# Kernel tuning notes

Hardware: AMD Instinct MI355X
Metric: run time of the kernel (lower is better)

Reference implementation:

```python
import jax, jax.numpy as jnp
import numpy as np

EMBED = 512
HEADS = 8
HEAD_DIM = EMBED // HEADS
SCALE_BASE = 512
NEG = -1e9


def xpos_apply(x, offset, downscale):
    # x: [(b h), L, d]
    L, d = x.shape[1], x.shape[2]
    min_pos = -(L + offset) // 2
    max_pos = L + offset + min_pos
    base = (jnp.arange(0, d, 2, dtype=jnp.float32) + 0.4 * d) / (1.4 * d)      # [d/2]
    power = jnp.arange(min_pos, max_pos, dtype=jnp.float32) / SCALE_BASE        # [L']
    scale = base[None, :] ** power[:, None]                                     # [L', d/2]
    half = d // 2
    inv_freq = 1.0 / (10000.0 ** (jnp.arange(half, dtype=jnp.float32) / half))
    sinusoid = jnp.arange(scale.shape[0], dtype=jnp.float32)[:, None] * inv_freq[None, :]
    sin, cos = jnp.sin(sinusoid), jnp.cos(sinusoid)
    # keep last L rows (no-op when offset == 0)
    scale, sin, cos = scale[-L:], sin[-L:], cos[-L:]
    if downscale:
        scale = 1.0 / scale
    sin2 = jnp.repeat(sin * scale, 2, axis=-1)   # duplicate_interleave -> [L, d]
    cos2 = jnp.repeat(cos * scale, 2, axis=-1)
    x1, x2 = x[..., ::2], x[..., 1::2]
    rot = jnp.stack([-x2, x1], axis=-1).reshape(x.shape)  # rotate_every_two
    return x * cos2[None] + rot * sin2[None]


def split_heads(x, b, L):
    # 'b l (h d) -> (b h) l d'
    return x.reshape(b, L, HEADS, HEAD_DIM).transpose(0, 2, 1, 3).reshape(b * HEADS, L, HEAD_DIM)


def setup_inputs() -> dict:
    key = jax.random.key(0)
    ks = jax.random.split(key, 12)
    b, L = 4, 2048
    inp = {
        'query': jax.random.normal(ks[0], (b, L, EMBED), jnp.float32),
        'key': jax.random.normal(ks[1], (b, L, EMBED), jnp.float32),
        'value': jax.random.normal(ks[2], (b, L, EMBED), jnp.float32),
        'key_padding_mask': jnp.zeros((b, L), jnp.bool_),
        'attn_mask': jnp.where(jnp.tril(jnp.ones((L, L), jnp.bool_)), 0.0, NEG).astype(jnp.float32),
    }
    s = 1.0 / np.sqrt(EMBED)
    inp['Wq'] = jax.random.normal(ks[3], (EMBED, EMBED), jnp.float32) * s
    inp['bq'] = jnp.zeros((EMBED,), jnp.float32)
    inp['Wk'] = jax.random.normal(ks[4], (EMBED, EMBED), jnp.float32) * s
    inp['bk'] = jnp.zeros((EMBED,), jnp.float32)
    inp['Wv'] = jax.random.normal(ks[5], (EMBED, EMBED), jnp.float32) * s
    inp['bv'] = jnp.zeros((EMBED,), jnp.float32)
    inp['Wo'] = jax.random.normal(ks[6], (EMBED, EMBED), jnp.float32) * s
    inp['bo'] = jnp.zeros((EMBED,), jnp.float32)
    return inp


def reference(query, key, value, key_padding_mask, attn_mask, Wq, bq, Wk, bk, Wv, bv, Wo, bo):
    b, L, _ = query.shape
    q = split_heads(query @ Wq.T + bq, b, L)
    k = split_heads(key @ Wk.T + bk, b, L)
    v = split_heads(value @ Wv.T + bv, b, L)
    k = xpos_apply(k, 0, True)
    q = xpos_apply(q, 0, False)
    q = q * (HEAD_DIM ** -0.5)
    aw = jnp.einsum('btd,bsd->bts', q, k)                 # [(b h), t, s]
    aw = jnp.nan_to_num(aw) + attn_mask[None]
    aw = aw.reshape(b, HEADS, L, L)
    aw = jnp.where(key_padding_mask[:, None, None, :], jnp.finfo(aw.dtype).min, aw)
    aw = aw.reshape(b * HEADS, L, L)
    probs = jax.nn.softmax(aw.astype(jnp.float32), axis=-1).astype(aw.dtype)
    attn = jnp.einsum('bts,bsd->btd', probs, v)           # [(b h), t, d]
    attn = attn.reshape(b, HEADS, L, HEAD_DIM).transpose(0, 2, 1, 3).reshape(b, L, EMBED)
    return attn @ Wo.T + bo
```

## Files before the change

kernel.cpp:

```cpp
#include <hip/hip_runtime.h>
#include <hip/hip_bf16.h>

typedef __bf16 bf16x2 __attribute__((ext_vector_type(2)));
typedef __bf16 bf16x4 __attribute__((ext_vector_type(4)));
typedef __bf16 bf16x8 __attribute__((ext_vector_type(8)));
typedef float  f32x4  __attribute__((ext_vector_type(4)));

#define SEQ    2048
#define EMB    512
#define NHEAD  8
#define HD     64
#define NBATCH 4
#define MROWS  (NBATCH*SEQ)
#define QSCALE 0.18033688011112042f
#define INV2PI 0.15915494309189535f
#define TWOPI  6.28318530717958648f
#define NEGFREQ (-0.41524101186092028f)

__device__ __forceinline__ f32x4 mfma16(bf16x8 a, bf16x8 b, f32x4 c) {
  return __builtin_amdgcn_mfma_f32_16x16x32_bf16(a, b, c, 0, 0, 0);
}

typedef __attribute__((address_space(1))) const void gv_t;
typedef __attribute__((address_space(3))) void lv_t;
__device__ __forceinline__ void async16(const void* g, void* l) {
  __builtin_amdgcn_global_load_lds((gv_t*)g, (lv_t*)l, 16, 0, 0);
}

__global__ __launch_bounds__(256) void conv_kernel(const float* __restrict__ q,
                                                   const float* __restrict__ k,
                                                   const float* __restrict__ v,
                                                   __bf16* __restrict__ Qf,
                                                   __bf16* __restrict__ Kf,
                                                   __bf16* __restrict__ Vf) {
  const int z = blockIdx.y;
  const float* src = (z == 0) ? q : (z == 1) ? k : v;
  __bf16* dst = (z == 0) ? Qf : (z == 1) ? Kf : Vf;
  const size_t i8 = ((size_t)blockIdx.x * 256 + threadIdx.x) * 8;
  const float4 fa = ((const float4*)(src + i8))[0];
  const float4 fb = ((const float4*)(src + i8))[1];
  bf16x8 h = { (__bf16)fa.x, (__bf16)fa.y, (__bf16)fa.z, (__bf16)fa.w,
               (__bf16)fb.x, (__bf16)fb.y, (__bf16)fb.z, (__bf16)fb.w };
  *(bf16x8*)(dst + i8) = h;
}

__device__ __forceinline__ void gemm_main(const __bf16* __restrict__ A,
                                          const float* __restrict__ W,
                                          __bf16* As, __bf16* Bs,
                                          f32x4 (&acc)[4][4], int m0, int n0) {
  const int tid = threadIdx.x;
  const int wid = tid >> 6, lane = tid & 63;
  const int quad = lane >> 4, l16 = lane & 15;
  const int srow = lane >> 3;
  const int sxor = ((lane & 7) ^ srow) * 8;
  const int wm = (wid >> 1) * 64, wn = (wid & 1) * 64;

  #pragma unroll
  for (int i = 0; i < 4; ++i)
    #pragma unroll
    for (int j = 0; j < 4; ++j) acc[i][j] = (f32x4)(0.0f);

  for (int k0 = 0; k0 < 512; k0 += 64) {
    __syncthreads();
    #pragma unroll
    for (int ii = 0; ii < 4; ++ii) {
      const int r8 = wid * 32 + ii * 8;
      async16(A + (size_t)(m0 + r8 + srow) * 512 + k0 + sxor, &As[r8 * 64]);
    }
    {
      const int row = tid >> 1, c0 = (tid & 1) << 5;
      const float* src = W + (size_t)(n0 + row) * 512 + k0 + c0;
      __bf16* dst = Bs + row * 72 + c0;
      #pragma unroll
      for (int j = 0; j < 4; ++j) {
        const float4 fa = ((const float4*)src)[2 * j];
        const float4 fb = ((const float4*)src)[2 * j + 1];
        bf16x8 h = { (__bf16)fa.x, (__bf16)fa.y, (__bf16)fa.z, (__bf16)fa.w,
                     (__bf16)fb.x, (__bf16)fb.y, (__bf16)fb.z, (__bf16)fb.w };
        *((bf16x8*)(dst + 8 * j)) = h;
      }
    }
    __syncthreads();
    #pragma unroll
    for (int ks = 0; ks < 2; ++ks) {
      bf16x8 af[4], bfr[4];
      #pragma unroll
      for (int i = 0; i < 4; ++i)
        af[i] = *(const bf16x8*)&As[(wm + i * 16 + l16) * 64 +
                                    (((quad + ks * 4) ^ (l16 & 7)) * 8)];
      #pragma unroll
      for (int j = 0; j < 4; ++j)
        bfr[j] = *(const bf16x8*)&Bs[(wn + j * 16 + l16) * 72 + ks * 32 + quad * 8];
      #pragma unroll
      for (int i = 0; i < 4; ++i)
        #pragma unroll
        for (int j = 0; j < 4; ++j)
          acc[i][j] = mfma16(af[i], bfr[j], acc[i][j]);
    }
  }
}

__global__ __launch_bounds__(256) void gemm_proj_kernel(
    const __bf16* __restrict__ Qf, const __bf16* __restrict__ Kf, const __bf16* __restrict__ Vf,
    const float* __restrict__ wq, const float* __restrict__ wk, const float* __restrict__ wv,
    const float* __restrict__ bq, const float* __restrict__ bk, const float* __restrict__ bv,
    __bf16* __restrict__ Qx, __bf16* __restrict__ Kx, __bf16* __restrict__ Vt) {
  __shared__ __align__(16) char smem[34816];
  __bf16* As = (__bf16*)smem;
  __bf16* Bs = (__bf16*)(smem + 16384);
  __bf16* T  = (__bf16*)smem;

  const int z = blockIdx.z;
  const __bf16* A = (z == 0) ? Qf : (z == 1) ? Kf : Vf;
  const float* W  = (z == 0) ? wq : (z == 1) ? wk : wv;
  const float* bias = (z == 0) ? bq : (z == 1) ? bk : bv;
  const int m0 = blockIdx.y * 128, n0 = blockIdx.x * 128;

  f32x4 acc[4][4];
  gemm_main(A, W, As, Bs, acc, m0, n0);

  const int tid = threadIdx.x;
  const int wid = tid >> 6, lane = tid & 63;
  const int quad = lane >> 4, l16 = lane & 15;
  const int wm = (wid >> 1) * 64, wn = (wid & 1) * 64;

  __syncthreads();

  if (z == 2) {
    #pragma unroll
    for (int j = 0; j < 4; ++j) {
      const float bval = bias[n0 + wn + j * 16 + l16];
      #pragma unroll
      for (int i = 0; i < 4; ++i) {
        bf16x4 p = { (__bf16)(acc[i][j][0] + bval), (__bf16)(acc[i][j][1] + bval),
                     (__bf16)(acc[i][j][2] + bval), (__bf16)(acc[i][j][3] + bval) };
        *(bf16x4*)&T[(wn + j * 16 + l16) * 136 + wm + i * 16 + quad * 4] = p;
      }
    }
    __syncthreads();
    const int nrow = tid >> 1, mh = (tid & 1) << 6;
    bf16x8 vv[8];
    #pragma unroll
    for (int u = 0; u < 8; ++u) vv[u] = *(const bf16x8*)&T[nrow * 136 + mh + u * 8];
    const int n = n0 + nrow, h = n >> 6, d = n & 63;
    const int bb = m0 >> 11, lb2 = (m0 & 2047) + mh;
    __bf16* dst = Vt + ((size_t)(bb * 8 + h) * 64 + d) * 2048 + lb2;
    #pragma unroll
    for (int u = 0; u < 8; ++u) *(bf16x8*)(dst + u * 8) = vv[u];
  } else {
    #pragma unroll
    for (int j = 0; j < 4; ++j) {
      const float bval = bias[n0 + wn + j * 16 + l16];
      #pragma unroll
      for (int i = 0; i < 4; ++i)
        #pragma unroll
        for (int r = 0; r < 4; ++r)
          T[(wm + i * 16 + quad * 4 + r) * 136 + wn + j * 16 + l16] =
              (__bf16)(acc[i][j][r] + bval);
    }
    __syncthreads();
    const int lrow = tid >> 1, half = tid & 1;
    const int gm = m0 + lrow, l = gm & 2047, bb = gm >> 11;
    const int h = (n0 >> 6) + half;
    bf16x8 vv[8];
    #pragma unroll
    for (int u = 0; u < 8; ++u)
      vv[u] = *(const bf16x8*)&T[lrow * 136 + half * 64 + u * 8];
    bf16x8 ov[8];
    const float lf = (float)l;
    const float pw = (lf - 1024.0f) * (1.0f / 512.0f);
    const float qs = (z == 0) ? QSCALE : 1.0f;
    #pragma unroll
    for (int i = 0; i < 32; ++i) {
      const float x1 = (float)vv[i >> 2][(2 * i) & 7];
      const float x2 = (float)vv[i >> 2][(2 * i + 1) & 7];
      const float lb = __log2f((2.0f * i + 25.6f) * (1.0f / 89.6f));
      const float e  = (z == 0) ? (pw * lb) : (-pw * lb);
      const float sc = __builtin_amdgcn_exp2f(e) * qs;
      const float ang = lf * __builtin_amdgcn_exp2f((float)i * NEGFREQ);
      float rev = ang * INV2PI;
      rev -= floorf(rev);
      const float ar = rev * TWOPI;
      const float sn = __sinf(ar) * sc;
      const float cs = __cosf(ar) * sc;
      ov[i >> 2][(2 * i) & 7]     = (__bf16)(x1 * cs - x2 * sn);
      ov[i >> 2][(2 * i + 1) & 7] = (__bf16)(x2 * cs + x1 * sn);
    }
    __bf16* dst = ((z == 0) ? Qx : Kx) + ((size_t)(bb * 8 + h) * 2048 + l) * 64;
    #pragma unroll
    for (int u = 0; u < 8; ++u) *(bf16x8*)(dst + u * 8) = ov[u];
  }
}

__global__ __launch_bounds__(256) void gemm_out_kernel(
    const __bf16* __restrict__ A, const float* __restrict__ W,
    const float* __restrict__ bias, float* __restrict__ C) {
  __shared__ __align__(16) char smem[34816];
  __bf16* As = (__bf16*)smem;
  __bf16* Bs = (__bf16*)(smem + 16384);
  const int m0 = blockIdx.y * 128, n0 = blockIdx.x * 128;
  f32x4 acc[4][4];
  gemm_main(A, W, As, Bs, acc, m0, n0);
  const int tid = threadIdx.x;
  const int wid = tid >> 6, lane = tid & 63;
  const int quad = lane >> 4, l16 = lane & 15;
  const int wm = (wid >> 1) * 64, wn = (wid & 1) * 64;
  #pragma unroll
  for (int j = 0; j < 4; ++j) {
    const int n = n0 + wn + j * 16 + l16;
    const float bval = bias[n];
    #pragma unroll
    for (int i = 0; i < 4; ++i)
      #pragma unroll
      for (int r = 0; r < 4; ++r)
        C[(size_t)(m0 + wm + i * 16 + quad * 4 + r) * 512 + n] = acc[i][j][r] + bval;
  }
}

__global__ __launch_bounds__(256, 3) void flash_kernel(const __bf16* __restrict__ Qx,
                                                       const __bf16* __restrict__ Kx,
                                                       const __bf16* __restrict__ Vt,
                                                       const unsigned char* __restrict__ kpm,
                                                       __bf16* __restrict__ Oa) {
  __shared__ __align__(16) __bf16 Qs[128 * HD];
  __shared__ __align__(16) __bf16 Ks[64 * HD];
  __shared__ __align__(16) __bf16 Vs[64 * HD];
  __shared__ __align__(16) __bf16 Ps[4][32 * 72];
  __shared__ __align__(16) unsigned char kpmS[2048];

  const int tid = threadIdx.x;
  const int wid = tid >> 6;
  const int lane = tid & 63;
  const int quad = lane >> 4;
  const int l16 = lane & 15;
  const int l7 = l16 & 7;
  const int srow = lane >> 3;
  const int sxor = ((lane & 7) ^ srow) * 8;
  const int bh = blockIdx.x;
  const int b = bh >> 3, h = bh & 7;
  const int y = blockIdx.y;
  const int qt = (y < 8) ? (15 - y) : (y - 8);
  const int q0 = qt * 128;
  const int nkv = 2 * qt + 2;

  const __bf16* Qbase = Qx + (size_t)bh * (SEQ * HD);
  const __bf16* Kbase = Kx + (size_t)bh * (SEQ * HD);
  const __bf16* Vbase = Vt + (size_t)bh * (HD * SEQ);
  __bf16* Pw = &Ps[wid][0];

  #pragma unroll
  for (int ii = 0; ii < 4; ++ii) {
    const int r0 = wid * 32 + ii * 8;
    async16(Qbase + (size_t)(q0 + r0 + srow) * HD + sxor, &Qs[r0 * HD]);
  }
  if (wid < 2) async16(kpm + b * SEQ + tid * 16, &kpmS[tid * 16]);
  #pragma unroll
  for (int ii = 0; ii < 2; ++ii) {
    const int r0 = wid * 16 + ii * 8;
    async16(Kbase + (size_t)(r0 + srow) * HD + sxor, &Ks[r0 * HD]);
    async16(Vbase + (size_t)(r0 + srow) * SEQ + sxor, &Vs[r0 * HD]);
  }
  __syncthreads();

  bf16x8 qf[2][2];
  #pragma unroll
  for (int ks = 0; ks < 2; ++ks)
    #pragma unroll
    for (int c = 0; c < 2; ++c)
      qf[ks][c] = *(const bf16x8*)&Qs[(wid * 32 + c * 16 + l16) * HD +
                                      (((quad + ks * 4) ^ l7) * 8)];

  f32x4 o[4][2];
  #pragma unroll
  for (int db = 0; db < 4; ++db)
    #pragma unroll
    for (int c = 0; c < 2; ++c) o[db][c] = (f32x4)(0.0f);
  float m_run[2] = { -3.0e38f, -3.0e38f };
  float l_run[2] = { 0.0f, 0.0f };
  const int myq0 = q0 + wid * 32 + l16;

  for (int kvt = 0; kvt < nkv; ++kvt) {
    f32x4 s[4][2];
    #pragma unroll
    for (int nb = 0; nb < 4; ++nb)
      #pragma unroll
      for (int c = 0; c < 2; ++c) s[nb][c] = (f32x4)(0.0f);
    #pragma unroll
    for (int ks = 0; ks < 2; ++ks) {
      bf16x8 kf[4];
      #pragma unroll
      for (int nb = 0; nb < 4; ++nb)
        kf[nb] = *(const bf16x8*)&Ks[(nb * 16 + l16) * HD + (((quad + ks * 4) ^ l7) * 8)];
      #pragma unroll
      for (int nb = 0; nb < 4; ++nb)
        #pragma unroll
        for (int c = 0; c < 2; ++c)
          s[nb][c] = mfma16(kf[nb], qf[ks][c], s[nb][c]);
    }

    if (kvt * 64 + 63 > q0 + wid * 32) {
      #pragma unroll
      for (int c = 0; c < 2; ++c) {
        const int myq = myq0 + c * 16;
        #pragma unroll
        for (int nb = 0; nb < 4; ++nb)
          #pragma unroll
          for (int r = 0; r < 4; ++r)
            if (kvt * 64 + nb * 16 + quad * 4 + r > myq) s[nb][c][r] = -1e30f;
      }
    }
    #pragma unroll
    for (int nb = 0; nb < 4; ++nb) {
      const unsigned pk = *(const unsigned*)&kpmS[kvt * 64 + nb * 16 + quad * 4];
      if (pk) {
        #pragma unroll
        for (int c = 0; c < 2; ++c) {
          if (pk & 0x000000FFu) s[nb][c][0] = -1e30f;
          if (pk & 0x0000FF00u) s[nb][c][1] = -1e30f;
          if (pk & 0x00FF0000u) s[nb][c][2] = -1e30f;
          if (pk & 0xFF000000u) s[nb][c][3] = -1e30f;
        }
      }
    }

    float alpha[2];
    #pragma unroll
    for (int c = 0; c < 2; ++c) {
      float mx = s[0][c][0];
      #pragma unroll
      for (int nb = 0; nb < 4; ++nb)
        #pragma unroll
        for (int r = 0; r < 4; ++r) mx = fmaxf(mx, s[nb][c][r]);
      mx = fmaxf(mx, __shfl_xor(mx, 16));
      mx = fmaxf(mx, __shfl_xor(mx, 32));
      const float m_new = fmaxf(m_run[c], mx);
      alpha[c] = __builtin_amdgcn_exp2f(m_run[c] - m_new);
      m_run[c] = m_new;
      float ssum = 0.0f;
      #pragma unroll
      for (int nb = 0; nb < 4; ++nb) {
        #pragma unroll
        for (int r = 0; r < 4; ++r) {
          const float p = __builtin_amdgcn_exp2f(s[nb][c][r] - m_new);
          s[nb][c][r] = p;
          ssum += p;
        }
      }
      ssum += __shfl_xor(ssum, 16);
      ssum += __shfl_xor(ssum, 32);
      l_run[c] = l_run[c] * alpha[c] + ssum;
    }

    #pragma unroll
    for (int c = 0; c < 2; ++c)
      #pragma unroll
      for (int nb = 0; nb < 4; ++nb) {
        bf16x4 p4 = { (__bf16)s[nb][c][0], (__bf16)s[nb][c][1],
                      (__bf16)s[nb][c][2], (__bf16)s[nb][c][3] };
        *(bf16x4*)&Pw[(c * 16 + l16) * 72 + nb * 16 + quad * 4] = p4;
      }
    #pragma unroll
    for (int db = 0; db < 4; ++db)
      #pragma unroll
      for (int c = 0; c < 2; ++c) o[db][c] *= alpha[c];

    #pragma unroll
    for (int ks = 0; ks < 2; ++ks) {
      bf16x8 pf[2];
      #pragma unroll
      for (int c = 0; c < 2; ++c)
        pf[c] = *(const bf16x8*)&Pw[(c * 16 + l16) * 72 + ks * 32 + quad * 8];
      #pragma unroll
      for (int db = 0; db < 4; ++db) {
        const bf16x8 vf = *(const bf16x8*)&Vs[(db * 16 + l16) * HD +
                                              (((quad + ks * 4) ^ l7) * 8)];
        #pragma unroll
        for (int c = 0; c < 2; ++c)
          o[db][c] = mfma16(vf, pf[c], o[db][c]);
      }
    }

    __syncthreads();
    if (kvt + 1 < nkv) {
      const int kvn = kvt + 1;
      #pragma unroll
      for (int ii = 0; ii < 2; ++ii) {
        const int r0 = wid * 16 + ii * 8;
        async16(Kbase + (size_t)(kvn * 64 + r0 + srow) * HD + sxor, &Ks[r0 * HD]);
        async16(Vbase + (size_t)(r0 + srow) * SEQ + kvn * 64 + sxor, &Vs[r0 * HD]);
      }
    }
    __syncthreads();
  }

  #pragma unroll
  for (int c = 0; c < 2; ++c) {
    const float inv_l = 1.0f / l_run[c];
    #pragma unroll
    for (int db = 0; db < 4; ++db) {
      bf16x4 t4 = { (__bf16)(o[db][c][0] * inv_l), (__bf16)(o[db][c][1] * inv_l),
                    (__bf16)(o[db][c][2] * inv_l), (__bf16)(o[db][c][3] * inv_l) };
      *(bf16x4*)&Pw[(c * 16 + l16) * 72 + db * 16 + quad * 4] = t4;
    }
  }
  #pragma unroll
  for (int ii = 0; ii < 4; ++ii) {
    const int qr = ii * 8 + srow;
    const bf16x8 ovv = *(const bf16x8*)&Pw[qr * 72 + (lane & 7) * 8];
    *(bf16x8*)(Oa + (((size_t)b * SEQ + q0 + wid * 32 + qr) * NHEAD + h) * HD +
               (lane & 7) * 8) = ovv;
  }
}

extern "C" void kernel_launch(void* const* d_in, const int* in_sizes, int n_in,
                              void* d_out, int out_size, void* d_ws, size_t ws_size,
                              hipStream_t stream) {
  (void)in_sizes; (void)n_in; (void)out_size; (void)ws_size;
  const float* query = (const float*)d_in[0];
  const float* key   = (const float*)d_in[1];
  const float* value = (const float*)d_in[2];
  const unsigned char* kpm = (const unsigned char*)d_in[3];
  const float* Wq = (const float*)d_in[5];
  const float* bq = (const float*)d_in[6];
  const float* Wk = (const float*)d_in[7];
  const float* bk = (const float*)d_in[8];
  const float* Wv = (const float*)d_in[9];
  const float* bv = (const float*)d_in[10];
  const float* Wo = (const float*)d_in[11];
  const float* bo = (const float*)d_in[12];
  float* out = (float*)d_out;

  char* ws = (char*)d_ws;
  const size_t SZ = (size_t)MROWS * EMB * 2;
  __bf16* Qf = (__bf16*)(ws);
  __bf16* Kf = (__bf16*)(ws + SZ);
  __bf16* Vf = (__bf16*)(ws + 2 * SZ);
  __bf16* Qx = (__bf16*)(ws + 3 * SZ);
  __bf16* Kx = (__bf16*)(ws + 4 * SZ);
  __bf16* Vt = (__bf16*)(ws + 5 * SZ);
  __bf16* Oa = Qf;

  conv_kernel<<<dim3(2048, 3), dim3(256), 0, stream>>>(query, key, value, Qf, Kf, Vf);
  gemm_proj_kernel<<<dim3(4, 64, 3), dim3(256), 0, stream>>>(
      Qf, Kf, Vf, Wq, Wk, Wv, bq, bk, bv, Qx, Kx, Vt);
  flash_kernel<<<dim3(32, 16), dim3(256), 0, stream>>>(Qx, Kx, Vt, kpm, Oa);
  gemm_out_kernel<<<dim3(4, 64), dim3(256), 0, stream>>>(Oa, Wo, bo, out);
}
```

Measured before the change: 239.3 us.

## Split flash attention into single-wave blocks reading K/V directly from global

Replaces the 4-wave block with shared-memory K/V staging by single-wavefront blocks, each handling two 32-row query tiles paired from opposite ends of the causal range so work per block is balanced. K, V, Q and the padding mask are now loaded straight from global memory into registers, with no LDS staging and no block barriers. This removes synchronization and LDS copies and raises the block count, but K/V tiles are no longer shared across waves, so global/L2 traffic rises and global loads go unswizzled and non-prefetched. It also drops the async double-load overlap.

```diff
diff --git a/kernel.cpp b/kernel.cpp
--- a/kernel.cpp
+++ b/kernel.cpp
@@ -217,198 +217,170 @@
   }
 }
 
-__global__ __launch_bounds__(256, 3) void flash_kernel(const __bf16* __restrict__ Qx,
-                                                       const __bf16* __restrict__ Kx,
-                                                       const __bf16* __restrict__ Vt,
-                                                       const unsigned char* __restrict__ kpm,
-                                                       __bf16* __restrict__ Oa) {
-  __shared__ __align__(16) __bf16 Qs[128 * HD];
-  __shared__ __align__(16) __bf16 Ks[64 * HD];
-  __shared__ __align__(16) __bf16 Vs[64 * HD];
-  __shared__ __align__(16) __bf16 Ps[4][32 * 72];
-  __shared__ __align__(16) unsigned char kpmS[2048];
-
-  const int tid = threadIdx.x;
-  const int wid = tid >> 6;
-  const int lane = tid & 63;
+__global__ __launch_bounds__(64) void flash_kernel(const __bf16* __restrict__ Qx,
+                                                   const __bf16* __restrict__ Kx,
+                                                   const __bf16* __restrict__ Vt,
+                                                   const unsigned char* __restrict__ kpm,
+                                                   __bf16* __restrict__ Oa) {
+  __shared__ __align__(16) __bf16 Pw[32 * 72];
+
+  const int lane = threadIdx.x;
   const int quad = lane >> 4;
   const int l16 = lane & 15;
-  const int l7 = l16 & 7;
-  const int srow = lane >> 3;
-  const int sxor = ((lane & 7) ^ srow) * 8;
   const int bh = blockIdx.x;
   const int b = bh >> 3, h = bh & 7;
-  const int y = blockIdx.y;
-  const int qt = (y < 8) ? (15 - y) : (y - 8);
-  const int q0 = qt * 128;
-  const int nkv = 2 * qt + 2;
+  const int w = blockIdx.y;
 
   const __bf16* Qbase = Qx + (size_t)bh * (SEQ * HD);
   const __bf16* Kbase = Kx + (size_t)bh * (SEQ * HD);
   const __bf16* Vbase = Vt + (size_t)bh * (HD * SEQ);
-  __bf16* Pw = &Ps[wid][0];
-
-  #pragma unroll
-  for (int ii = 0; ii < 4; ++ii) {
-    const int r0 = wid * 32 + ii * 8;
-    async16(Qbase + (size_t)(q0 + r0 + srow) * HD + sxor, &Qs[r0 * HD]);
-  }
-  if (wid < 2) async16(kpm + b * SEQ + tid * 16, &kpmS[tid * 16]);
-  #pragma unroll
-  for (int ii = 0; ii < 2; ++ii) {
-    const int r0 = wid * 16 + ii * 8;
-    async16(Kbase + (size_t)(r0 + srow) * HD + sxor, &Ks[r0 * HD]);
-    async16(Vbase + (size_t)(r0 + srow) * SEQ + sxor, &Vs[r0 * HD]);
-  }
-  __syncthreads();
-
-  bf16x8 qf[2][2];
-  #pragma unroll
-  for (int ks = 0; ks < 2; ++ks)
-    #pragma unroll
-    for (int c = 0; c < 2; ++c)
-      qf[ks][c] = *(const bf16x8*)&Qs[(wid * 32 + c * 16 + l16) * HD +
-                                      (((quad + ks * 4) ^ l7) * 8)];
-
-  f32x4 o[4][2];
-  #pragma unroll
-  for (int db = 0; db < 4; ++db)
-    #pragma unroll
-    for (int c = 0; c < 2; ++c) o[db][c] = (f32x4)(0.0f);
-  float m_run[2] = { -3.0e38f, -3.0e38f };
-  float l_run[2] = { 0.0f, 0.0f };
-  const int myq0 = q0 + wid * 32 + l16;
-
-  for (int kvt = 0; kvt < nkv; ++kvt) {
-    f32x4 s[4][2];
-    #pragma unroll
-    for (int nb = 0; nb < 4; ++nb)
-      #pragma unroll
-      for (int c = 0; c < 2; ++c) s[nb][c] = (f32x4)(0.0f);
-    #pragma unroll
-    for (int ks = 0; ks < 2; ++ks) {
-      bf16x8 kf[4];
+  const unsigned char* kpb = kpm + b * SEQ;
+
+  #pragma unroll 1
+  for (int phase = 0; phase < 2; ++phase) {
+    const int qb2 = phase ? w : (63 - w);
+    const int q0 = qb2 * 32;
+    const int nkv = (qb2 >> 1) + 1;
+
+    bf16x8 qf[2][2];
+    #pragma unroll
+    for (int ks = 0; ks < 2; ++ks)
+      #pragma unroll
+      for (int c = 0; c < 2; ++c)
+        qf[ks][c] = *(const bf16x8*)(Qbase + (size_t)(q0 + c * 16 + l16) * HD +
+                                     ks * 32 + quad * 8);
+
+    f32x4 o[4][2];
+    #pragma unroll
+    for (int db = 0; db < 4; ++db)
+      #pragma unroll
+      for (int c = 0; c < 2; ++c) o[db][c] = (f32x4)(0.0f);
+    float m_run[2] = { -3.0e38f, -3.0e38f };
+    float l_run[2] = { 0.0f, 0.0f };
+
+    #pragma unroll 1
+    for (int kvt = 0; kvt < nkv; ++kvt) {
+      const int kv0 = kvt * 64;
+
+      f32x4 s[4][2];
       #pragma unroll
       for (int nb = 0; nb < 4; ++nb)
-        kf[nb] = *(const bf16x8*)&Ks[(nb * 16 + l16) * HD + (((quad + ks * 4) ^ l7) * 8)];
-      #pragma unroll
-      for (int nb = 0; nb < 4; ++nb)
+        #pragma unroll
+        for (int c = 0; c < 2; ++c) s[nb][c] = (f32x4)(0.0f);
+      #pragma unroll
+      for (int ks = 0; ks < 2; ++ks) {
+        bf16x8 kf[4];
+        #pragma unroll
+        for (int nb = 0; nb < 4; ++nb)
+          kf[nb] = *(const bf16x8*)(Kbase + (size_t)(kv0 + nb * 16 + l16) * HD +
+                                    ks * 32 + quad * 8);
+        #pragma unroll
+        for (int nb = 0; nb < 4; ++nb)
+          #pragma unroll
+          for (int c = 0; c < 2; ++c)
+            s[nb][c] = mfma16(kf[nb], qf[ks][c], s[nb][c]);
+      }
+
+      if (kvt == nkv - 1) {
+        #pragma unroll
+        for (int c = 0; c < 2; ++c) {
+          const int myq = q0 + c * 16 + l16;
+          #pragma unroll
+          for (int nb = 0; nb < 4; ++nb)
+            #pragma unroll
+            for (int r = 0; r < 4; ++r)
+              if (kv0 + nb * 16 + quad * 4 + r > myq) s[nb][c][r] = -1e30f;
+        }
+      }
+      #pragma unroll
+      for (int nb = 0; nb < 4; ++nb) {
+        const unsigned pk = *(const unsigned*)(kpb + kv0 + nb * 16 + quad * 4);
+        if (pk) {
+          #pragma unroll
+          for (int c = 0; c < 2; ++c) {
+            if (pk & 0x000000FFu) s[nb][c][0] = -1e30f;
+            if (pk & 0x0000FF00u) s[nb][c][1] = -1e30f;
+            if (pk & 0x00FF0000u) s[nb][c][2] = -1e30f;
+            if (pk & 0xFF000000u) s[nb][c][3] = -1e30f;
+          }
+        }
+      }
+
+      float alpha[2];
+      #pragma unroll
+      for (int c = 0; c < 2; ++c) {
+        float mx = s[0][c][0];
+        #pragma unroll
+        for (int nb = 0; nb < 4; ++nb)
+          #pragma unroll
+          for (int r = 0; r < 4; ++r) mx = fmaxf(mx, s[nb][c][r]);
+        mx = fmaxf(mx, __shfl_xor(mx, 16));
+        mx = fmaxf(mx, __shfl_xor(mx, 32));
+        const float m_new = fmaxf(m_run[c], mx);
+        alpha[c] = __builtin_amdgcn_exp2f(m_run[c] - m_new);
+        m_run[c] = m_new;
+        float ssum = 0.0f;
+        #pragma unroll
+        for (int nb = 0; nb < 4; ++nb) {
+          #pragma unroll
+          for (int r = 0; r < 4; ++r) {
+            const float p = __builtin_amdgcn_exp2f(s[nb][c][r] - m_new);
+            s[nb][c][r] = p;
+            ssum += p;
+          }
+        }
+        ssum += __shfl_xor(ssum, 16);
+        ssum += __shfl_xor(ssum, 32);
+        l_run[c] = l_run[c] * alpha[c] + ssum;
+      }
+
+      #pragma unroll
+      for (int c = 0; c < 2; ++c)
+        #pragma unroll
+        for (int nb = 0; nb < 4; ++nb) {
+          bf16x4 p4 = { (__bf16)s[nb][c][0], (__bf16)s[nb][c][1],
+                        (__bf16)s[nb][c][2], (__bf16)s[nb][c][3] };
+          *(bf16x4*)&Pw[(c * 16 + l16) * 72 + nb * 16 + quad * 4] = p4;
+        }
+      #pragma unroll
+      for (int db = 0; db < 4; ++db)
+        #pragma unroll
+        for (int c = 0; c < 2; ++c) o[db][c] *= alpha[c];
+
+      #pragma unroll
+      for (int ks = 0; ks < 2; ++ks) {
+        bf16x8 pf[2];
         #pragma unroll
         for (int c = 0; c < 2; ++c)
-          s[nb][c] = mfma16(kf[nb], qf[ks][c], s[nb][c]);
-    }
-
-    if (kvt * 64 + 63 > q0 + wid * 32) {
-      #pragma unroll
-      for (int c = 0; c < 2; ++c) {
-        const int myq = myq0 + c * 16;
-        #pragma unroll
-        for (int nb = 0; nb < 4; ++nb)
-          #pragma unroll
-          for (int r = 0; r < 4; ++r)
-            if (kvt * 64 + nb * 16 + quad * 4 + r > myq) s[nb][c][r] = -1e30f;
-      }
-    }
-    #pragma unroll
-    for (int nb = 0; nb < 4; ++nb) {
-      const unsigned pk = *(const unsigned*)&kpmS[kvt * 64 + nb * 16 + quad * 4];
-      if (pk) {
-        #pragma unroll
-        for (int c = 0; c < 2; ++c) {
-          if (pk & 0x000000FFu) s[nb][c][0] = -1e30f;
-          if (pk & 0x0000FF00u) s[nb][c][1] = -1e30f;
-          if (pk & 0x00FF0000u) s[nb][c][2] = -1e30f;
-          if (pk & 0xFF000000u) s[nb][c][3] = -1e30f;
+          pf[c] = *(const bf16x8*)&Pw[(c * 16 + l16) * 72 + ks * 32 + quad * 8];
+        #pragma unroll
+        for (int db = 0; db < 4; ++db) {
+          const bf16x8 vf = *(const bf16x8*)(Vbase + (size_t)(db * 16 + l16) * SEQ +
+                                             kv0 + ks * 32 + quad * 8);
+          #pragma unroll
+          for (int c = 0; c < 2; ++c)
+            o[db][c] = mfma16(vf, pf[c], o[db][c]);
         }
       }
     }
 
-    float alpha[2];
     #pragma unroll
     for (int c = 0; c < 2; ++c) {
-      float mx = s[0][c][0];
-      #pragma unroll
-      for (int nb = 0; nb < 4; ++nb)
-        #pragma unroll
-        for (int r = 0; r < 4; ++r) mx = fmaxf(mx, s[nb][c][r]);
-      mx = fmaxf(mx, __shfl_xor(mx, 16));
-      mx = fmaxf(mx, __shfl_xor(mx, 32));
-      const float m_new = fmaxf(m_run[c], mx);
-      alpha[c] = __builtin_amdgcn_exp2f(m_run[c] - m_new);
-      m_run[c] = m_new;
-      float ssum = 0.0f;
-      #pragma unroll
-      for (int nb = 0; nb < 4; ++nb) {
-        #pragma unroll
-        for (int r = 0; r < 4; ++r) {
-          const float p = __builtin_amdgcn_exp2f(s[nb][c][r] - m_new);
-          s[nb][c][r] = p;
-          ssum += p;
-        }
-      }
-      ssum += __shfl_xor(ssum, 16);
-      ssum += __shfl_xor(ssum, 32);
-      l_run[c] = l_run[c] * alpha[c] + ssum;
-    }
-
-    #pragma unroll
-    for (int c = 0; c < 2; ++c)
-      #pragma unroll
-      for (int nb = 0; nb < 4; ++nb) {
-        bf16x4 p4 = { (__bf16)s[nb][c][0], (__bf16)s[nb][c][1],
-                      (__bf16)s[nb][c][2], (__bf16)s[nb][c][3] };
-        *(bf16x4*)&Pw[(c * 16 + l16) * 72 + nb * 16 + quad * 4] = p4;
-      }
-    #pragma unroll
-    for (int db = 0; db < 4; ++db)
-      #pragma unroll
-      for (int c = 0; c < 2; ++c) o[db][c] *= alpha[c];
-
-    #pragma unroll
-    for (int ks = 0; ks < 2; ++ks) {
-      bf16x8 pf[2];
-      #pragma unroll
-      for (int c = 0; c < 2; ++c)
-        pf[c] = *(const bf16x8*)&Pw[(c * 16 + l16) * 72 + ks * 32 + quad * 8];
+      const float inv_l = 1.0f / l_run[c];
       #pragma unroll
       for (int db = 0; db < 4; ++db) {
-        const bf16x8 vf = *(const bf16x8*)&Vs[(db * 16 + l16) * HD +
-                                              (((quad + ks * 4) ^ l7) * 8)];
-        #pragma unroll
-        for (int c = 0; c < 2; ++c)
-          o[db][c] = mfma16(vf, pf[c], o[db][c]);
-      }
-    }
-
-    __syncthreads();
-    if (kvt + 1 < nkv) {
-      const int kvn = kvt + 1;
-      #pragma unroll
-      for (int ii = 0; ii < 2; ++ii) {
-        const int r0 = wid * 16 + ii * 8;
-        async16(Kbase + (size_t)(kvn * 64 + r0 + srow) * HD + sxor, &Ks[r0 * HD]);
-        async16(Vbase + (size_t)(r0 + srow) * SEQ + kvn * 64 + sxor, &Vs[r0 * HD]);
-      }
-    }
-    __syncthreads();
-  }
-
-  #pragma unroll
-  for (int c = 0; c < 2; ++c) {
-    const float inv_l = 1.0f / l_run[c];
-    #pragma unroll
-    for (int db = 0; db < 4; ++db) {
-      bf16x4 t4 = { (__bf16)(o[db][c][0] * inv_l), (__bf16)(o[db][c][1] * inv_l),
-                    (__bf16)(o[db][c][2] * inv_l), (__bf16)(o[db][c][3] * inv_l) };
-      *(bf16x4*)&Pw[(c * 16 + l16) * 72 + db * 16 + quad * 4] = t4;
-    }
-  }
-  #pragma unroll
-  for (int ii = 0; ii < 4; ++ii) {
-    const int qr = ii * 8 + srow;
-    const bf16x8 ovv = *(const bf16x8*)&Pw[qr * 72 + (lane & 7) * 8];
-    *(bf16x8*)(Oa + (((size_t)b * SEQ + q0 + wid * 32 + qr) * NHEAD + h) * HD +
-               (lane & 7) * 8) = ovv;
+        bf16x4 t4 = { (__bf16)(o[db][c][0] * inv_l), (__bf16)(o[db][c][1] * inv_l),
+                      (__bf16)(o[db][c][2] * inv_l), (__bf16)(o[db][c][3] * inv_l) };
+        *(bf16x4*)&Pw[(c * 16 + l16) * 72 + db * 16 + quad * 4] = t4;
+      }
+    }
+    #pragma unroll
+    for (int ii = 0; ii < 4; ++ii) {
+      const int qr = ii * 8 + (lane >> 3);
+      const bf16x8 ovv = *(const bf16x8*)&Pw[qr * 72 + (lane & 7) * 8];
+      *(bf16x8*)(Oa + (((size_t)b * SEQ + q0 + qr) * NHEAD + h) * HD +
+                 (lane & 7) * 8) = ovv;
+    }
   }
 }
 
@@ -443,6 +415,6 @@
   conv_kernel<<<dim3(2048, 3), dim3(256), 0, stream>>>(query, key, value, Qf, Kf, Vf);
   gemm_proj_kernel<<<dim3(4, 64, 3), dim3(256), 0, stream>>>(
       Qf, Kf, Vf, Wq, Wk, Wv, bq, bk, bv, Qx, Kx, Vt);
-  flash_kernel<<<dim3(32, 16), dim3(256), 0, stream>>>(Qx, Kx, Vt, kpm, Oa);
+  flash_kernel<<<dim3(32, 64), dim3(64), 0, stream>>>(Qx, Kx, Vt, kpm, Oa);
   gemm_out_kernel<<<dim3(4, 64), dim3(256), 0, stream>>>(Oa, Wo, bo, out);
 }
```

Result: slower. 334.2 us (+39.7%).
